# Kernel tuning notes

Hardware: AMD Instinct MI355X
Metric: run time of the kernel (lower is better)

## Reference

```python
import jax, jax.numpy as jnp
import numpy as np
import itertools, math

MODES = 10
PHOTONS = 5
_IN_MODES_NP = np.arange(0, MODES, 2)  # input_state = [1,0,1,0,...]: photons in even modes
IN_MODES = jnp.asarray(_IN_MODES_NP)

# ---- Ryser's formula constants for 5x5 permanents (2^5 = 32 column subsets) ----
P = PHOTONS
_SUBS = np.array([[(s >> j) & 1 for j in range(P)] for s in range(1 << P)], dtype=np.float32)
_SIGNS = np.array([(-1.0) ** (P - bin(s).count('1')) for s in range(1 << P)], dtype=np.float32)
SUBS_C = jnp.asarray(_SUBS).astype(jnp.complex64)   # (32, P)
SIGNS = jnp.asarray(_SIGNS)                          # (32,)


def permanents(A):
    """Batched permanent via Ryser. A: (..., P, P) complex64 -> (...,) complex64."""
    # row sums over each column subset: (..., 32, P)
    rs = jnp.einsum('...rc,sc->...sr', A, SUBS_C)
    prods = jnp.prod(rs, axis=-1)            # (..., 32)
    return jnp.sum(prods * SIGNS, axis=-1)


def circuit_probs(theta, UL, UR, rows, norm):
    """Photonic circuit: U = UL @ diag(exp(i*theta)) @ UR, single photons in IN_MODES.
    theta: (N, m) real phases; rows: (K, P) output-row multisets; norm: 1/prod(occ!).
    Returns (N, K) Fock-state probabilities."""
    D = jnp.exp(1j * theta.astype(jnp.complex64))             # (N, m)
    U = jnp.einsum('ij,nj,jk->nik', UL, D, UR)                # (N, m, m)
    Ucols = U[:, :, IN_MODES]                                  # (N, m, P) input columns
    sub = Ucols[:, rows, :]                                    # (N, K, P, P)
    pm = permanents(sub)                                       # (N, K)
    return (pm.real ** 2 + pm.imag ** 2) * norm


def _cx(W):
    return (W[..., 0] + 1j * W[..., 1]).astype(jnp.complex64)


def setup_inputs() -> dict:
    key = jax.random.key(0)
    ks = jax.random.split(key, 8)
    N, input_dim, m, p = 256, 784, MODES, PHOTONS
    x = jax.random.normal(ks[0], (N, input_dim), jnp.float32)
    W_down = jax.random.normal(ks[1], (m, input_dim), jnp.float32) / np.sqrt(input_dim)
    b_down = jnp.zeros((m,), jnp.float32)

    def rand_unitary(k):
        a = jax.random.normal(k, (m, m, 2), jnp.float32)
        q, _ = jnp.linalg.qr((a[..., 0] + 1j * a[..., 1]).astype(jnp.complex64))
        return jnp.stack([q.real, q.imag], axis=-1).astype(jnp.float32)

    U1L, U1R, UfL, UfR = (rand_unitary(ks[i]) for i in range(2, 6))

    # circuit 1 keys: no_bunching -> C(10,5)=252 single-occupancy states
    keys1 = np.array(list(itertools.combinations(range(m), p)), dtype=np.int32)  # (252, 5)
    occ1 = np.zeros((len(keys1), m), dtype=np.float32)
    occ1[np.arange(len(keys1))[:, None], keys1] = 1.0   # occupancy mask (keys >= 1)
    # final circuit keys: bunching allowed -> C(14,5)=2002 multisets of modes
    rows2_np = np.array(list(itertools.combinations_with_replacement(range(m), p)), dtype=np.int32)
    norm2_np = np.array(
        [1.0 / np.prod([math.factorial(int(c)) for c in np.bincount(r, minlength=m)]) for r in rows2_np],
        dtype=np.float32)

    W_out = jax.random.normal(ks[6], (2, len(rows2_np)), jnp.float32) / np.sqrt(len(rows2_np))
    b_out = jnp.zeros((2,), jnp.float32)
    return {
        'x': x, 'W_down': W_down, 'b_down': b_down,
        'U1L': U1L, 'U1R': U1R, 'UfL': UfL, 'UfR': UfR,
        'W_out': W_out, 'b_out': b_out,
        'mask1': jnp.asarray(occ1), 'norm2': jnp.asarray(norm2_np),
        'rows1': jnp.asarray(keys1), 'rows2': jnp.asarray(rows2_np),
    }


def reference(x, W_down, b_down, U1L, U1R, UfL, UfR, W_out, b_out, mask1, norm2, rows1, rows2):
    h = x @ W_down.T + b_down            # downscaling_layer: (N, m)
    theta = h / jnp.pi                   # DivideByPi
    # quantum circuit 1 (no_bunching=True -> postselected/renormalized subspace)
    p1 = circuit_probs(theta, _cx(U1L), _cx(U1R), rows1, 1.0)       # (N, 252)
    p1 = p1 / jnp.sum(p1, axis=-1, keepdims=True)
    e1 = p1 @ mask1                       # marginalize_photon_presence: (N, m)
    # final quantum circuit (full Fock distribution, E=1)
    pf = circuit_probs(e1, _cx(UfL), _cx(UfR), rows2, norm2)        # (N, 2002)
    return pf @ W_out.T + b_out           # output_layer logits (N, 2)
```

## Files before the change

### kernel.cpp

```cpp
#include <hip/hip_runtime.h>
#include <hip/hip_bf16.h>


__device__ __forceinline__ float2 cxmul(float2 a, float2 b) {
    float2 r;
    r.x = fmaf(a.x, b.x, -(a.y * b.y));
    r.y = fmaf(a.x, b.y, a.y * b.x);
    return r;
}
__device__ __forceinline__ float2 cadd(float2 a, float2 b) {
    return make_float2(a.x + b.x, a.y + b.y);
}

struct BTab { int v[16][7]; };
constexpr BTab make_btab() {
    BTab t{};
    for (int n = 0; n < 16; ++n)
        for (int k = 0; k < 7; ++k) {
            if (k == 0) t.v[n][k] = 1;
            else if (n == 0) t.v[n][k] = 0;
            else t.v[n][k] = t.v[n - 1][k - 1] + t.v[n - 1][k];
        }
    return t;
}
constexpr BTab BT = make_btab();

constexpr int rank3c(int a, int b, int c) {
    return BT.v[a][1] + BT.v[b + 1][2] + BT.v[c + 2][3];
}
constexpr int rank4c(int a, int b, int c, int d) {
    return BT.v[a][1] + BT.v[b + 1][2] + BT.v[c + 2][3] + BT.v[d + 3][4];
}

struct T3 { unsigned pm[220]; float inv[220]; };
constexpr T3 gen3() {
    T3 t{};
    for (int a = 0; a <= 9; ++a)
        for (int b = a; b <= 9; ++b)
            for (int c = b; c <= 9; ++c) {
                const int R = rank3c(a, b, c);
                t.pm[R] = (unsigned)a | ((unsigned)b << 4) | ((unsigned)c << 8);
                int f = 1;
                if (a == b && b == c) f = 6;
                else if (a == b || b == c) f = 2;
                t.inv[R] = 1.0f / (float)f;
            }
    return t;
}
__device__ constexpr T3 T3T = gen3();

struct T4 { unsigned e[715][4]; };
constexpr T4 gen4() {
    T4 t{};
    for (int a = 0; a <= 9; ++a)
     for (int b = a; b <= 9; ++b)
      for (int c = b; c <= 9; ++c)
       for (int d = c; d <= 9; ++d) {
           const int R = rank4c(a, b, c, d);
           const int m[4] = {a, b, c, d};
           for (int j = 0; j < 4; ++j) {
               if (j > 0 && m[j] == m[j - 1]) { t.e[R][j] = 0u; continue; }
               int p[3]; int q = 0;
               for (int i = 0; i < 4; ++i) if (i != j) p[q++] = m[i];
               t.e[R][j] = ((unsigned)rank3c(p[0], p[1], p[2]) << 4)
                         | (unsigned)m[j] | 0x80000000u;
           }
       }
    return t;
}
__device__ constexpr T4 T4T = gen4();

struct T5A { unsigned e[252][5]; unsigned cm[252]; };
constexpr T5A gen5a() {
    T5A t{};
    int p = 0;
    for (int a = 0; a <= 9; ++a)
     for (int b = a + 1; b <= 9; ++b)
      for (int c = b + 1; c <= 9; ++c)
       for (int d = c + 1; d <= 9; ++d)
        for (int g = d + 1; g <= 9; ++g) {
            const int m[5] = {a, b, c, d, g};
            for (int j = 0; j < 5; ++j) {
                int q4[4]; int q = 0;
                for (int i = 0; i < 5; ++i) if (i != j) q4[q++] = m[i];
                t.e[p][j] = ((unsigned)rank4c(q4[0], q4[1], q4[2], q4[3]) << 4)
                          | (unsigned)m[j] | 0x80000000u;
            }
            t.cm[p] = (1u << a) | (1u << b) | (1u << c) | (1u << d) | (1u << g);
            ++p;
        }
    return t;
}
__device__ constexpr T5A T5AT = gen5a();

struct T5B { unsigned e[2002][5]; float fact[2002]; };
constexpr T5B gen5b() {
    T5B t{};
    int p = 0;
    for (int a = 0; a <= 9; ++a)
     for (int b = a; b <= 9; ++b)
      for (int c = b; c <= 9; ++c)
       for (int d = c; d <= 9; ++d)
        for (int g = d; g <= 9; ++g) {
            const int m[5] = {a, b, c, d, g};
            for (int j = 0; j < 5; ++j) {
                if (j > 0 && m[j] == m[j - 1]) { t.e[p][j] = 0u; continue; }
                int q4[4]; int q = 0;
                for (int i = 0; i < 5; ++i) if (i != j) q4[q++] = m[i];
                t.e[p][j] = ((unsigned)rank4c(q4[0], q4[1], q4[2], q4[3]) << 4)
                          | (unsigned)m[j] | 0x80000000u;
            }
            int f = 1, cnt = 1;
            for (int i = 1; i < 5; ++i) { cnt = (m[i] == m[i - 1]) ? cnt + 1 : 1; f *= cnt; }
            t.fact[p] = (float)f;
            ++p;
        }
    return t;
}
__device__ constexpr T5B T5BT = gen5b();

__device__ __forceinline__ float2 dp_acc(float2 acc, unsigned e, const float2* pbuf,
                                         const float2* B, int col) {
    if (e & 0x80000000u) {
        float2 p = pbuf[(e >> 4) & 0x3FFu];
        float2 b = B[(e & 15u) * 5 + col];
        acc.x = fmaf(b.x, p.x, acc.x);
        acc.x = fmaf(-b.y, p.y, acc.x);
        acc.y = fmaf(b.x, p.y, acc.y);
        acc.y = fmaf(b.y, p.x, acc.y);
    }
    return acc;
}

__global__ __launch_bounds__(1024) void k_fused(
    const float* __restrict__ x, const float* __restrict__ Wd, const float* __restrict__ bd,
    const float* __restrict__ U1L, const float* __restrict__ U1R,
    const float* __restrict__ UfL, const float* __restrict__ UfR,
    const float* __restrict__ Wout, const float* __restrict__ bout,
    float* __restrict__ out)
{
    const int n    = blockIdx.x;
    const int tid  = threadIdx.x;
    const int lane = tid & 63;
    const int wid  = tid >> 6;

    __shared__ float2 Bsh[50];
    __shared__ float2 st3[220];
    __shared__ float2 st4[715];
    __shared__ float  p1s[252];
    __shared__ float2 Dsh[10];
    __shared__ float  fred[16][2];

    unsigned pm3 = 0u; float inv3 = 0.f;
    if (tid < 220) { pm3 = T3T.pm[tid]; inv3 = T3T.inv[tid]; }
    unsigned e4[4] = {0u, 0u, 0u, 0u};
    if (tid < 715) {
#pragma unroll
        for (int j = 0; j < 4; ++j) e4[j] = T4T.e[tid][j];
    }
    unsigned e5a[5] = {0u, 0u, 0u, 0u, 0u};
    if (tid < 252) {
#pragma unroll
        for (int j = 0; j < 5; ++j) e5a[j] = T5AT.e[tid][j];
    }
    unsigned e5b0[5];
#pragma unroll
    for (int j = 0; j < 5; ++j) e5b0[j] = T5BT.e[tid][j];
    const bool has_p1 = (tid + 1024) < 2002;
    unsigned e5b1[5] = {0u, 0u, 0u, 0u, 0u};
    if (has_p1) {
#pragma unroll
        for (int j = 0; j < 5; ++j) e5b1[j] = T5BT.e[tid + 1024][j];
    }
    const float fact0 = T5BT.fact[tid];
    const float fact1 = has_p1 ? T5BT.fact[tid + 1024] : 0.f;
    const float w0a = Wout[tid];
    const float w1a = Wout[2002 + tid];
    const float w0b = has_p1 ? Wout[tid + 1024] : 0.f;
    const float w1b = has_p1 ? Wout[2002 + tid + 1024] : 0.f;
    unsigned cmw[4] = {0u, 0u, 0u, 0u};
    if (wid < 10) {
#pragma unroll
        for (int t = 0; t < 4; ++t) {
            const int p = lane + t * 64;
            cmw[t] = (p < 252) ? T5AT.cm[p] : 0u;
        }
    }
    const int q   = tid >> 1;
    const int par = tid & 1;
    const int bi  = q / 5;
    const int bk  = 2 * (q % 5);
    const int jb  = par * 5;
    float2 u1l[5], u1r[5], ufl[5], ufr[5];
    if (tid < 100) {
#pragma unroll
        for (int t = 0; t < 5; ++t) {
            const int j = jb + t;
            u1l[t] = make_float2(U1L[(bi * 10 + j) * 2], U1L[(bi * 10 + j) * 2 + 1]);
            u1r[t] = make_float2(U1R[(j * 10 + bk) * 2], U1R[(j * 10 + bk) * 2 + 1]);
            ufl[t] = make_float2(UfL[(bi * 10 + j) * 2], UfL[(bi * 10 + j) * 2 + 1]);
            ufr[t] = make_float2(UfR[(j * 10 + bk) * 2], UfR[(j * 10 + bk) * 2 + 1]);
        }
    }

    if (wid < 10) {
        const float* xr = x + n * 784;
        const float* wr = Wd + wid * 784;
        float s0 = 0.f, s1 = 0.f, s2 = 0.f, s3 = 0.f;
#pragma unroll
        for (int t = 0; t < 12; t += 4) {
            s0 = fmaf(xr[lane + t * 64],       wr[lane + t * 64],       s0);
            s1 = fmaf(xr[lane + (t + 1) * 64], wr[lane + (t + 1) * 64], s1);
            s2 = fmaf(xr[lane + (t + 2) * 64], wr[lane + (t + 2) * 64], s2);
            s3 = fmaf(xr[lane + (t + 3) * 64], wr[lane + (t + 3) * 64], s3);
        }
        if (lane < 16) s0 = fmaf(xr[lane + 768], wr[lane + 768], s0);
        float s = (s0 + s1) + (s2 + s3);
#pragma unroll
        for (int off = 32; off > 0; off >>= 1) s += __shfl_xor(s, off, 64);
        if (lane == 0) {
            float h = s + bd[wid];
            float sn, cs;
            __sincosf(h * 0.31830988618379067154f, &sn, &cs);
            Dsh[wid] = make_float2(cs, sn);
        }
    }
    __syncthreads();

    if (tid < 100) {
        float2 a = make_float2(0.f, 0.f);
#pragma unroll
        for (int t = 0; t < 5; ++t) {
            float2 tt = cxmul(cxmul(u1l[t], Dsh[jb + t]), u1r[t]);
            a.x += tt.x; a.y += tt.y;
        }
        a.x += __shfl_xor(a.x, 1, 64);
        a.y += __shfl_xor(a.y, 1, 64);
        if (par == 0) Bsh[q] = a;
    }
    __syncthreads();

    if (tid < 220) {
        const int a = pm3 & 15u, b = (pm3 >> 4) & 15u, c = (pm3 >> 8) & 15u;
        const float2 A0 = Bsh[a * 5 + 0], A1 = Bsh[a * 5 + 1], A2 = Bsh[a * 5 + 2];
        const float2 B0 = Bsh[b * 5 + 0], B1 = Bsh[b * 5 + 1], B2 = Bsh[b * 5 + 2];
        const float2 C0 = Bsh[c * 5 + 0], C1 = Bsh[c * 5 + 1], C2 = Bsh[c * 5 + 2];
        float2 r = cxmul(A0, cadd(cxmul(B1, C2), cxmul(C1, B2)));
        r = cadd(r, cxmul(B0, cadd(cxmul(A1, C2), cxmul(C1, A2))));
        r = cadd(r, cxmul(C0, cadd(cxmul(A1, B2), cxmul(B1, A2))));
        st3[tid] = make_float2(r.x * inv3, r.y * inv3);
    }
    __syncthreads();
    if (tid < 715) {
        float2 a = make_float2(0.f, 0.f);
#pragma unroll
        for (int j = 0; j < 4; ++j) a = dp_acc(a, e4[j], st3, Bsh, 3);
        st4[tid] = a;
    }
    __syncthreads();
    if (tid < 252) {
        float2 a = make_float2(0.f, 0.f);
#pragma unroll
        for (int j = 0; j < 5; ++j) a = dp_acc(a, e5a[j], st4, Bsh, 4);
        p1s[tid] = fmaf(a.x, a.x, a.y * a.y);
    }
    __syncthreads();

    if (wid < 10) {
        float sm = 0.f, st = 0.f;
#pragma unroll
        for (int t = 0; t < 4; ++t) {
            const int p = lane + t * 64;
            if (p < 252) {
                const float pv = p1s[p];
                sm = fmaf(pv, (float)((cmw[t] >> wid) & 1u), sm);
                st += pv;
            }
        }
#pragma unroll
        for (int off = 32; off > 0; off >>= 1) {
            sm += __shfl_xor(sm, off, 64);
            st += __shfl_xor(st, off, 64);
        }
        if (lane == 0) {
            float e = sm / st;
            float sn, cs;
            __sincosf(e, &sn, &cs);
            Dsh[wid] = make_float2(cs, sn);
        }
    }
    __syncthreads();

    if (tid < 100) {
        float2 a = make_float2(0.f, 0.f);
#pragma unroll
        for (int t = 0; t < 5; ++t) {
            float2 tt = cxmul(cxmul(ufl[t], Dsh[jb + t]), ufr[t]);
            a.x += tt.x; a.y += tt.y;
        }
        a.x += __shfl_xor(a.x, 1, 64);
        a.y += __shfl_xor(a.y, 1, 64);
        if (par == 0) Bsh[q] = a;
    }
    __syncthreads();

    if (tid < 220) {
        const int a = pm3 & 15u, b = (pm3 >> 4) & 15u, c = (pm3 >> 8) & 15u;
        const float2 A0 = Bsh[a * 5 + 0], A1 = Bsh[a * 5 + 1], A2 = Bsh[a * 5 + 2];
        const float2 B0 = Bsh[b * 5 + 0], B1 = Bsh[b * 5 + 1], B2 = Bsh[b * 5 + 2];
        const float2 C0 = Bsh[c * 5 + 0], C1 = Bsh[c * 5 + 1], C2 = Bsh[c * 5 + 2];
        float2 r = cxmul(A0, cadd(cxmul(B1, C2), cxmul(C1, B2)));
        r = cadd(r, cxmul(B0, cadd(cxmul(A1, C2), cxmul(C1, A2))));
        r = cadd(r, cxmul(C0, cadd(cxmul(A1, B2), cxmul(B1, A2))));
        st3[tid] = make_float2(r.x * inv3, r.y * inv3);
    }
    __syncthreads();
    if (tid < 715) {
        float2 a = make_float2(0.f, 0.f);
#pragma unroll
        for (int j = 0; j < 4; ++j) a = dp_acc(a, e4[j], st3, Bsh, 3);
        st4[tid] = a;
    }
    __syncthreads();

    float f0 = 0.f, f1 = 0.f;
    {
        float2 a = make_float2(0.f, 0.f);
#pragma unroll
        for (int j = 0; j < 5; ++j) a = dp_acc(a, e5b0[j], st4, Bsh, 4);
        const float pf = fmaf(a.x, a.x, a.y * a.y) * fact0;
        f0 = fmaf(pf, w0a, f0);
        f1 = fmaf(pf, w1a, f1);
    }
    if (has_p1) {
        float2 a = make_float2(0.f, 0.f);
#pragma unroll
        for (int j = 0; j < 5; ++j) a = dp_acc(a, e5b1[j], st4, Bsh, 4);
        const float pf = fmaf(a.x, a.x, a.y * a.y) * fact1;
        f0 = fmaf(pf, w0b, f0);
        f1 = fmaf(pf, w1b, f1);
    }
#pragma unroll
    for (int off = 32; off > 0; off >>= 1) {
        f0 += __shfl_xor(f0, off, 64);
        f1 += __shfl_xor(f1, off, 64);
    }
    if (lane == 0) { fred[wid][0] = f0; fred[wid][1] = f1; }
    __syncthreads();
    if (tid < 16) {
        float a0 = fred[tid][0];
        float a1 = fred[tid][1];
#pragma unroll
        for (int off = 8; off > 0; off >>= 1) {
            a0 += __shfl_xor(a0, off, 64);
            a1 += __shfl_xor(a1, off, 64);
        }
        if (tid == 0) {
            out[n * 2 + 0] = a0 + bout[0];
            out[n * 2 + 1] = a1 + bout[1];
        }
    }
}

extern "C" void kernel_launch(void* const* d_in, const int* in_sizes, int n_in,
                              void* d_out, int out_size, void* d_ws, size_t ws_size,
                              hipStream_t stream) {
    const float* x     = (const float*)d_in[0];
    const float* Wd    = (const float*)d_in[1];
    const float* bd    = (const float*)d_in[2];
    const float* U1L   = (const float*)d_in[3];
    const float* U1R   = (const float*)d_in[4];
    const float* UfL   = (const float*)d_in[5];
    const float* UfR   = (const float*)d_in[6];
    const float* Wout  = (const float*)d_in[7];
    const float* bout  = (const float*)d_in[8];
    float* out = (float*)d_out;

    hipLaunchKernelGGL(k_fused, dim3(256), dim3(1024), 0, stream,
                       x, Wd, bd, U1L, U1R, UfL, UfR, Wout, bout, out);
}
```

Baseline: 12.52 us.

## Compute 4x4 sub-permanents directly, dropping the 3x3 Laplace stage and a barrier

Replaces the two-stage Laplace expansion (3x3 permanents, then 4x4 built from them) with a direct 4x4 permanent computed from pairwise 2x2 permanents. For the first circuit it computes only the 210 distinct-row 4x4 minors instead of all 715 multiset ones. The B matrix is stored padded to 10 entries per row so rows can be read with float4 loads. This removes one __syncthreads per circuit and the st3 traffic, at the cost of more arithmetic per thread in the 4x4 stage.

```diff
diff --git a/kernel.cpp b/kernel.cpp
--- a/kernel.cpp
+++ b/kernel.cpp
@@ -25,54 +25,47 @@
 }
 constexpr BTab BT = make_btab();
 
-constexpr int rank3c(int a, int b, int c) {
-    return BT.v[a][1] + BT.v[b + 1][2] + BT.v[c + 2][3];
-}
-constexpr int rank4c(int a, int b, int c, int d) {
+constexpr int rank4m(int a, int b, int c, int d) {
     return BT.v[a][1] + BT.v[b + 1][2] + BT.v[c + 2][3] + BT.v[d + 3][4];
 }
-
-struct T3 { unsigned pm[220]; float inv[220]; };
-constexpr T3 gen3() {
-    T3 t{};
+constexpr int rank4s(int a, int b, int c, int d) {
+    return BT.v[a][1] + BT.v[b][2] + BT.v[c][3] + BT.v[d][4];
+}
+
+struct S4SQ { unsigned pm[210]; };
+constexpr S4SQ gen4sq() {
+    S4SQ t{};
     for (int a = 0; a <= 9; ++a)
-        for (int b = a; b <= 9; ++b)
-            for (int c = b; c <= 9; ++c) {
-                const int R = rank3c(a, b, c);
-                t.pm[R] = (unsigned)a | ((unsigned)b << 4) | ((unsigned)c << 8);
-                int f = 1;
-                if (a == b && b == c) f = 6;
-                else if (a == b || b == c) f = 2;
-                t.inv[R] = 1.0f / (float)f;
-            }
-    return t;
-}
-__device__ constexpr T3 T3T = gen3();
-
-struct T4 { unsigned e[715][4]; };
-constexpr T4 gen4() {
-    T4 t{};
+     for (int b = a + 1; b <= 9; ++b)
+      for (int c = b + 1; c <= 9; ++c)
+       for (int d = c + 1; d <= 9; ++d)
+           t.pm[rank4s(a, b, c, d)] =
+               (unsigned)a | ((unsigned)b << 4) | ((unsigned)c << 8) | ((unsigned)d << 12);
+    return t;
+}
+__device__ constexpr S4SQ S4SQT = gen4sq();
+
+struct S4MS { unsigned pm[715]; float inv[715]; };
+constexpr S4MS gen4ms() {
+    S4MS t{};
     for (int a = 0; a <= 9; ++a)
      for (int b = a; b <= 9; ++b)
       for (int c = b; c <= 9; ++c)
        for (int d = c; d <= 9; ++d) {
-           const int R = rank4c(a, b, c, d);
+           const int R = rank4m(a, b, c, d);
+           t.pm[R] = (unsigned)a | ((unsigned)b << 4) | ((unsigned)c << 8) | ((unsigned)d << 12);
            const int m[4] = {a, b, c, d};
-           for (int j = 0; j < 4; ++j) {
-               if (j > 0 && m[j] == m[j - 1]) { t.e[R][j] = 0u; continue; }
-               int p[3]; int q = 0;
-               for (int i = 0; i < 4; ++i) if (i != j) p[q++] = m[i];
-               t.e[R][j] = ((unsigned)rank3c(p[0], p[1], p[2]) << 4)
-                         | (unsigned)m[j] | 0x80000000u;
-           }
+           int f = 1, cnt = 1;
+           for (int i = 1; i < 4; ++i) { cnt = (m[i] == m[i - 1]) ? cnt + 1 : 1; f *= cnt; }
+           t.inv[R] = 1.0f / (float)f;
        }
     return t;
 }
-__device__ constexpr T4 T4T = gen4();
-
-struct T5A { unsigned e[252][5]; unsigned cm[252]; };
-constexpr T5A gen5a() {
-    T5A t{};
+__device__ constexpr S4MS S4MST = gen4ms();
+
+struct S5A { unsigned e[252][5]; unsigned cm[252]; };
+constexpr S5A gen5a() {
+    S5A t{};
     int p = 0;
     for (int a = 0; a <= 9; ++a)
      for (int b = a + 1; b <= 9; ++b)
@@ -83,15 +76,15 @@
             for (int j = 0; j < 5; ++j) {
                 int q4[4]; int q = 0;
                 for (int i = 0; i < 5; ++i) if (i != j) q4[q++] = m[i];
-                t.e[p][j] = ((unsigned)rank4c(q4[0], q4[1], q4[2], q4[3]) << 4)
-                          | (unsigned)m[j] | 0x80000000u;
+                t.e[p][j] = ((unsigned)rank4s(q4[0], q4[1], q4[2], q4[3]) << 4)
+                          | (unsigned)m[j];
             }
             t.cm[p] = (1u << a) | (1u << b) | (1u << c) | (1u << d) | (1u << g);
             ++p;
         }
     return t;
 }
-__device__ constexpr T5A T5AT = gen5a();
+__device__ constexpr S5A S5AT = gen5a();
 
 struct T5B { unsigned e[2002][5]; float fact[2002]; };
 constexpr T5B gen5b() {
@@ -107,7 +100,7 @@
                 if (j > 0 && m[j] == m[j - 1]) { t.e[p][j] = 0u; continue; }
                 int q4[4]; int q = 0;
                 for (int i = 0; i < 5; ++i) if (i != j) q4[q++] = m[i];
-                t.e[p][j] = ((unsigned)rank4c(q4[0], q4[1], q4[2], q4[3]) << 4)
+                t.e[p][j] = ((unsigned)rank4m(q4[0], q4[1], q4[2], q4[3]) << 4)
                           | (unsigned)m[j] | 0x80000000u;
             }
             int f = 1, cnt = 1;
@@ -119,17 +112,36 @@
 }
 __device__ constexpr T5B T5BT = gen5b();
 
-__device__ __forceinline__ float2 dp_acc(float2 acc, unsigned e, const float2* pbuf,
-                                         const float2* B, int col) {
-    if (e & 0x80000000u) {
-        float2 p = pbuf[(e >> 4) & 0x3FFu];
-        float2 b = B[(e & 15u) * 5 + col];
-        acc.x = fmaf(b.x, p.x, acc.x);
-        acc.x = fmaf(-b.y, p.y, acc.x);
-        acc.y = fmaf(b.x, p.y, acc.y);
-        acc.y = fmaf(b.y, p.x, acc.y);
-    }
-    return acc;
+__device__ __forceinline__ void ld_row(const float2* Bsh, int m, float2 (&R)[4]) {
+    const float4* p = (const float4*)(Bsh + m * 10);
+    const float4 lo = p[0];
+    const float4 hi = p[1];
+    R[0] = make_float2(lo.x, lo.y);
+    R[1] = make_float2(lo.z, lo.w);
+    R[2] = make_float2(hi.x, hi.y);
+    R[3] = make_float2(hi.z, hi.w);
+}
+__device__ __forceinline__ float2 p22(const float2 (&A)[4], const float2 (&B)[4], int i, int j) {
+    return cadd(cxmul(A[i], B[j]), cxmul(A[j], B[i]));
+}
+__device__ __forceinline__ float2 perm4f(const float2* Bsh, unsigned pk) {
+    const int r0 = pk & 15u, r1 = (pk >> 4) & 15u, r2 = (pk >> 8) & 15u, r3 = (pk >> 12) & 15u;
+    float2 A[4], B[4], C[4], D[4];
+    ld_row(Bsh, r0, A); ld_row(Bsh, r1, B);
+    ld_row(Bsh, r2, C); ld_row(Bsh, r3, D);
+    float2 t01 = p22(A, B, 0, 1), t23 = p22(A, B, 2, 3);
+    float2 t02 = p22(A, B, 0, 2), t13 = p22(A, B, 1, 3);
+    float2 t03 = p22(A, B, 0, 3), t12 = p22(A, B, 1, 2);
+    float2 u01 = p22(C, D, 0, 1), u23 = p22(C, D, 2, 3);
+    float2 u02 = p22(C, D, 0, 2), u13 = p22(C, D, 1, 3);
+    float2 u03 = p22(C, D, 0, 3), u12 = p22(C, D, 1, 2);
+    float2 r = cxmul(t01, u23);
+    r = cadd(r, cxmul(t02, u13));
+    r = cadd(r, cxmul(t03, u12));
+    r = cadd(r, cxmul(t12, u03));
+    r = cadd(r, cxmul(t13, u02));
+    r = cadd(r, cxmul(t23, u01));
+    return r;
 }
 
 __global__ __launch_bounds__(1024) void k_fused(
@@ -144,24 +156,20 @@
     const int lane = tid & 63;
     const int wid  = tid >> 6;
 
-    __shared__ float2 Bsh[50];
-    __shared__ float2 st3[220];
+    __shared__ float2 Bsh[100];
     __shared__ float2 st4[715];
     __shared__ float  p1s[252];
     __shared__ float2 Dsh[10];
     __shared__ float  fred[16][2];
 
-    unsigned pm3 = 0u; float inv3 = 0.f;
-    if (tid < 220) { pm3 = T3T.pm[tid]; inv3 = T3T.inv[tid]; }
-    unsigned e4[4] = {0u, 0u, 0u, 0u};
-    if (tid < 715) {
-#pragma unroll
-        for (int j = 0; j < 4; ++j) e4[j] = T4T.e[tid][j];
-    }
+    unsigned pm4sq = 0u;
+    if (tid < 210) pm4sq = S4SQT.pm[tid];
+    unsigned pm4ms = 0u; float inv4 = 0.f;
+    if (tid < 715) { pm4ms = S4MST.pm[tid]; inv4 = S4MST.inv[tid]; }
     unsigned e5a[5] = {0u, 0u, 0u, 0u, 0u};
     if (tid < 252) {
 #pragma unroll
-        for (int j = 0; j < 5; ++j) e5a[j] = T5AT.e[tid][j];
+        for (int j = 0; j < 5; ++j) e5a[j] = S5AT.e[tid][j];
     }
     unsigned e5b0[5];
 #pragma unroll
@@ -183,13 +191,14 @@
 #pragma unroll
         for (int t = 0; t < 4; ++t) {
             const int p = lane + t * 64;
-            cmw[t] = (p < 252) ? T5AT.cm[p] : 0u;
+            cmw[t] = (p < 252) ? S5AT.cm[p] : 0u;
         }
     }
     const int q   = tid >> 1;
     const int par = tid & 1;
     const int bi  = q / 5;
-    const int bk  = 2 * (q % 5);
+    const int bc  = q % 5;
+    const int bk  = 2 * bc;
     const int jb  = par * 5;
     float2 u1l[5], u1r[5], ufl[5], ufr[5];
     if (tid < 100) {
@@ -236,32 +245,24 @@
         }
         a.x += __shfl_xor(a.x, 1, 64);
         a.y += __shfl_xor(a.y, 1, 64);
-        if (par == 0) Bsh[q] = a;
-    }
-    __syncthreads();
-
-    if (tid < 220) {
-        const int a = pm3 & 15u, b = (pm3 >> 4) & 15u, c = (pm3 >> 8) & 15u;
-        const float2 A0 = Bsh[a * 5 + 0], A1 = Bsh[a * 5 + 1], A2 = Bsh[a * 5 + 2];
-        const float2 B0 = Bsh[b * 5 + 0], B1 = Bsh[b * 5 + 1], B2 = Bsh[b * 5 + 2];
-        const float2 C0 = Bsh[c * 5 + 0], C1 = Bsh[c * 5 + 1], C2 = Bsh[c * 5 + 2];
-        float2 r = cxmul(A0, cadd(cxmul(B1, C2), cxmul(C1, B2)));
-        r = cadd(r, cxmul(B0, cadd(cxmul(A1, C2), cxmul(C1, A2))));
-        r = cadd(r, cxmul(C0, cadd(cxmul(A1, B2), cxmul(B1, A2))));
-        st3[tid] = make_float2(r.x * inv3, r.y * inv3);
-    }
-    __syncthreads();
-    if (tid < 715) {
-        float2 a = make_float2(0.f, 0.f);
-#pragma unroll
-        for (int j = 0; j < 4; ++j) a = dp_acc(a, e4[j], st3, Bsh, 3);
-        st4[tid] = a;
-    }
+        if (par == 0) Bsh[bi * 10 + bc] = a;
+    }
+    __syncthreads();
+
+    if (tid < 210) st4[tid] = perm4f(Bsh, pm4sq);
     __syncthreads();
     if (tid < 252) {
         float2 a = make_float2(0.f, 0.f);
 #pragma unroll
-        for (int j = 0; j < 5; ++j) a = dp_acc(a, e5a[j], st4, Bsh, 4);
+        for (int j = 0; j < 5; ++j) {
+            const unsigned e = e5a[j];
+            const float2 p = st4[e >> 4];
+            const float2 b = Bsh[(e & 15u) * 10 + 4];
+            a.x = fmaf(b.x, p.x, a.x);
+            a.x = fmaf(-b.y, p.y, a.x);
+            a.y = fmaf(b.x, p.y, a.y);
+            a.y = fmaf(b.y, p.x, a.y);
+        }
         p1s[tid] = fmaf(a.x, a.x, a.y * a.y);
     }
     __syncthreads();
@@ -300,26 +301,13 @@
         }
         a.x += __shfl_xor(a.x, 1, 64);
         a.y += __shfl_xor(a.y, 1, 64);
-        if (par == 0) Bsh[q] = a;
-    }
-    __syncthreads();
-
-    if (tid < 220) {
-        const int a = pm3 & 15u, b = (pm3 >> 4) & 15u, c = (pm3 >> 8) & 15u;
-        const float2 A0 = Bsh[a * 5 + 0], A1 = Bsh[a * 5 + 1], A2 = Bsh[a * 5 + 2];
-        const float2 B0 = Bsh[b * 5 + 0], B1 = Bsh[b * 5 + 1], B2 = Bsh[b * 5 + 2];
-        const float2 C0 = Bsh[c * 5 + 0], C1 = Bsh[c * 5 + 1], C2 = Bsh[c * 5 + 2];
-        float2 r = cxmul(A0, cadd(cxmul(B1, C2), cxmul(C1, B2)));
-        r = cadd(r, cxmul(B0, cadd(cxmul(A1, C2), cxmul(C1, A2))));
-        r = cadd(r, cxmul(C0, cadd(cxmul(A1, B2), cxmul(B1, A2))));
-        st3[tid] = make_float2(r.x * inv3, r.y * inv3);
-    }
-    __syncthreads();
+        if (par == 0) Bsh[bi * 10 + bc] = a;
+    }
+    __syncthreads();
+
     if (tid < 715) {
-        float2 a = make_float2(0.f, 0.f);
-#pragma unroll
-        for (int j = 0; j < 4; ++j) a = dp_acc(a, e4[j], st3, Bsh, 3);
-        st4[tid] = a;
+        float2 r = perm4f(Bsh, pm4ms);
+        st4[tid] = make_float2(r.x * inv4, r.y * inv4);
     }
     __syncthreads();
 
@@ -327,7 +315,17 @@
     {
         float2 a = make_float2(0.f, 0.f);
 #pragma unroll
-        for (int j = 0; j < 5; ++j) a = dp_acc(a, e5b0[j], st4, Bsh, 4);
+        for (int j = 0; j < 5; ++j) {
+            const unsigned e = e5b0[j];
+            if (e & 0x80000000u) {
+                const float2 p = st4[(e >> 4) & 0x3FFu];
+                const float2 b = Bsh[(e & 15u) * 10 + 4];
+                a.x = fmaf(b.x, p.x, a.x);
+                a.x = fmaf(-b.y, p.y, a.x);
+                a.y = fmaf(b.x, p.y, a.y);
+                a.y = fmaf(b.y, p.x, a.y);
+            }
+        }
         const float pf = fmaf(a.x, a.x, a.y * a.y) * fact0;
         f0 = fmaf(pf, w0a, f0);
         f1 = fmaf(pf, w1a, f1);
@@ -335,7 +333,17 @@
     if (has_p1) {
         float2 a = make_float2(0.f, 0.f);
 #pragma unroll
-        for (int j = 0; j < 5; ++j) a = dp_acc(a, e5b1[j], st4, Bsh, 4);
+        for (int j = 0; j < 5; ++j) {
+            const unsigned e = e5b1[j];
+            if (e & 0x80000000u) {
+                const float2 p = st4[(e >> 4) & 0x3FFu];
+                const float2 b = Bsh[(e & 15u) * 10 + 4];
+                a.x = fmaf(b.x, p.x, a.x);
+                a.x = fmaf(-b.y, p.y, a.x);
+                a.y = fmaf(b.x, p.y, a.y);
+                a.y = fmaf(b.y, p.x, a.y);
+            }
+        }
         const float pf = fmaf(a.x, a.x, a.y * a.y) * fact1;
         f0 = fmaf(pf, w0b, f0);
         f1 = fmaf(pf, w1b, f1);
```

After: 12.45 us. About the same (-0.6%).
